# Performance work log

Hardware: AMD Instinct MI355X
Metric: run time of the kernel (lower is better)

Reference implementation:

```python
import jax, jax.numpy as jnp
import numpy as np

HEADS = 4
DIM_HEAD = 32
EPS = 1e-5


def setup_inputs() -> dict:
    key = jax.random.key(0)
    ks = jax.random.split(key, 4)
    B, dim, H, W = 8, 256, 128, 128
    hidden = HEADS * DIM_HEAD  # 128
    x = jax.random.normal(ks[0], (B, dim, H, W), dtype=jnp.float32)
    # 1x1 conv weights stored as [out_ch, in_ch]
    qkv_w = jax.random.normal(ks[1], (3 * hidden, dim), dtype=jnp.float32) * (1.0 / np.sqrt(dim))
    conv_w = jax.random.normal(ks[2], (dim, hidden), dtype=jnp.float32) * (1.0 / np.sqrt(hidden))
    conv_b = jax.random.normal(ks[3], (dim,), dtype=jnp.float32) * 0.01
    gamma = jnp.ones((dim,), dtype=jnp.float32)
    beta = jnp.zeros((dim,), dtype=jnp.float32)
    return {"x": x, "qkv_w": qkv_w, "conv_w": conv_w, "conv_b": conv_b,
            "gamma": gamma, "beta": beta}


def reference(x, qkv_w, conv_w, conv_b, gamma, beta):
    B, C, H, W = x.shape
    N = H * W
    scale = DIM_HEAD ** (-0.5)
    # qkv 1x1 conv -> [B, 3, heads, dim_head, N]
    qkv = jnp.einsum('oc,bchw->bohw', qkv_w, x).reshape(B, 3, HEADS, DIM_HEAD, N)
    q, k, v = qkv[:, 0], qkv[:, 1], qkv[:, 2]
    q = jax.nn.softmax(q, axis=-2) * scale   # softmax over dim_head axis
    k = jax.nn.softmax(k, axis=-1)           # softmax over spatial axis
    v = v / N
    # context = k @ v^T : [B, h, d, d]
    context = jnp.einsum('bhdn,bhen->bhde', k, v)
    # out = context @ q : [B, h, d, N]
    out = jnp.einsum('bhde,bhen->bhdn', context, q)
    out = out.reshape(B, HEADS * DIM_HEAD, H, W)
    # final 1x1 conv with bias
    y = jnp.einsum('oc,bchw->bohw', conv_w, out) + conv_b[None, :, None, None]
    # InstanceNorm2d(affine=True): per-sample per-channel over (H, W), biased var
    mean = jnp.mean(y, axis=(2, 3), keepdims=True)
    var = jnp.var(y, axis=(2, 3), keepdims=True)
    y = (y - mean) * jax.lax.rsqrt(var + EPS)
    return y * gamma[None, :, None, None] + beta[None, :, None, None]
```

## Files before the change

kernel.cpp:

```cpp
#include <hip/hip_runtime.h>
#include <math.h>

#define NPIX 16384
#define DIMC 256
#define BATCH 8
#define HEADS 4
#define DHEAD 32
#define HID 128
#define OQKV 384
#define EPS 1e-5f
#define SCALE 0.17677669529663687f

typedef _Float16 f16x8 __attribute__((ext_vector_type(8)));
typedef float f32x4 __attribute__((ext_vector_type(4)));

__device__ inline void gl_lds16(const void* g, void* l) {
    __builtin_amdgcn_global_load_lds(
        (const __attribute__((address_space(1))) unsigned*)g,
        (__attribute__((address_space(3))) unsigned*)l, 16, 0, 0);
}

__global__ __launch_bounds__(256) void prep_kernel(
    const float* __restrict__ qkv_w, const float* __restrict__ conv_w,
    _Float16* __restrict__ wh, _Float16* __restrict__ ch, float* __restrict__ zbuf)
{
    int i = blockIdx.x * 256 + threadIdx.x;
    if (i < 98304) wh[i] = (_Float16)qkv_w[i];
    else           ch[i - 98304] = (_Float16)conv_w[i - 98304];
    if (i < 37888) zbuf[i] = 0.f;
}

__global__ __launch_bounds__(256) void transpose_x(const float* __restrict__ x,
                                                   _Float16* __restrict__ xh)
{
    __shared__ float tile[64][65];
    int t = threadIdx.x;
    int n0 = blockIdx.x * 64;
    int c0 = blockIdx.y * 64;
    int b  = blockIdx.z;
    const float* xb = x + (long)b * DIMC * NPIX;
    #pragma unroll
    for (int it = 0; it < 4; it++) {
        int c  = it * 16 + (t >> 4);
        int n4 = (t & 15) * 4;
        float4 v = *(const float4*)&xb[(long)(c0 + c) * NPIX + n0 + n4];
        tile[c][n4] = v.x; tile[c][n4+1] = v.y; tile[c][n4+2] = v.z; tile[c][n4+3] = v.w;
    }
    __syncthreads();
    _Float16* xo = xh + (long)b * NPIX * DIMC;
    #pragma unroll
    for (int it = 0; it < 2; it++) {
        int n  = it * 32 + (t >> 3);
        int c8 = (t & 7) * 8;
        f16x8 o;
        #pragma unroll
        for (int k = 0; k < 8; k++) o[k] = (_Float16)tile[c8 + k][n];
        *(f16x8*)&xo[(long)(n0 + n) * DIMC + c0 + c8] = o;
    }
}

template<int K, int EPI>
__global__ __launch_bounds__(256) void gemm_h(
    const _Float16* __restrict__ A,
    const _Float16* __restrict__ Bm,
    _Float16* __restrict__ Cm,
    long bsB, long bsC, float* __restrict__ lnacc)
{
    __shared__ _Float16 smem[16384];
    _Float16* As = smem;
    _Float16* Bs = smem + 4096;
    const int t  = threadIdx.x;
    const int b  = blockIdx.x;
    const int m0 = blockIdx.y * 128;
    const int n0 = blockIdx.z * 128;
    const _Float16* Bb = Bm + (long)b * bsB;
    const int w = t >> 6, lane = t & 63;
    const int q = lane >> 4, l16 = lane & 15;
    const int mw = (w >> 1) * 64, nw = (w & 1) * 64;

    f32x4 acc[4][4] = {};

    for (int k0 = 0; k0 < K; k0 += 32) {
        #pragma unroll
        for (int is = 0; is < 2; is++) {
            int idx = is * 256 + t;
            int row = idx >> 2, kc = (idx & 3) * 8;
            gl_lds16(&A [(long)(m0 + row) * K + k0 + kc], &As[idx * 8]);
            gl_lds16(&Bb[(long)(n0 + row) * K + k0 + kc], &Bs[idx * 8]);
        }
        __syncthreads();
        f16x8 af[4], bf[4];
        #pragma unroll
        for (int i = 0; i < 4; i++) {
            af[i] = *(const f16x8*)&As[(mw + i * 16 + l16) * 32 + q * 8];
            bf[i] = *(const f16x8*)&Bs[(nw + i * 16 + l16) * 32 + q * 8];
        }
        #pragma unroll
        for (int i = 0; i < 4; i++)
            #pragma unroll
            for (int j = 0; j < 4; j++)
                acc[i][j] = __builtin_amdgcn_mfma_f32_16x16x32_f16(af[i], bf[j], acc[i][j], 0, 0, 0);
        __syncthreads();
    }

    _Float16* Cs = smem;
    #pragma unroll
    for (int i = 0; i < 4; i++) {
        #pragma unroll
        for (int j = 0; j < 4; j++) {
            #pragma unroll
            for (int r = 0; r < 4; r++) {
                int row = mw + i * 16 + q * 4 + r;
                int col = nw + j * 16 + l16;
                Cs[row * 128 + (col ^ ((row & 15) << 3))] = (_Float16)acc[i][j][r];
            }
        }
    }
    __syncthreads();
    _Float16* Cb = Cm + (long)b * bsC;
    #pragma unroll
    for (int it = 0; it < 8; it++) {
        int u = it * 256 + t;
        int row = u >> 4, cg = u & 15;
        f16x8 v8 = *(const f16x8*)&Cs[row * 128 + ((cg * 8) ^ ((row & 15) << 3))];
        *(f16x8*)&Cb[(long)(m0 + row) * NPIX + n0 + cg * 8] = v8;
        if (EPI) {
            float s = 0.f, sq = 0.f;
            #pragma unroll
            for (int k = 0; k < 8; k++) { float f = (float)v8[k]; s += f; sq += f * f; }
            #pragma unroll
            for (int off = 8; off > 0; off >>= 1) {
                s  += __shfl_down(s,  off, 16);
                sq += __shfl_down(sq, off, 16);
            }
            if ((t & 15) == 0) {
                int rg = b * DIMC + m0 + row;
                atomicAdd(&lnacc[rg * 2],     s);
                atomicAdd(&lnacc[rg * 2 + 1], sq);
            }
        }
    }
}

__global__ __launch_bounds__(256) void ctx_mfma(const _Float16* __restrict__ qkvh,
    float* __restrict__ ctx_raw, float* __restrict__ ksum)
{
    __shared__ float cbuf[4][1024];
    int t = threadIdx.x;
    int w = t >> 6, lane = t & 63;
    int q = lane >> 4, l16 = lane & 15;
    int bh = blockIdx.y, b = bh >> 2, h = bh & 3;
    const _Float16* kb = qkvh + ((long)b * OQKV + HID + h * DHEAD) * NPIX;
    const _Float16* vb = qkvh + ((long)b * OQKV + 2 * HID + h * DHEAD) * NPIX;
    long n0 = (long)blockIdx.x * 2048 + w * 512 + q * 8;

    f32x4 c00 = {}, c01 = {}, c10 = {}, c11 = {};
    float ks0 = 0.f, ks1 = 0.f;

    for (int s = 0; s < 16; s++) {
        long n = n0 + s * 32;
        f16x8 kf0 = *(const f16x8*)&kb[(long)l16 * NPIX + n];
        f16x8 kf1 = *(const f16x8*)&kb[(long)(16 + l16) * NPIX + n];
        f16x8 vf0 = *(const f16x8*)&vb[(long)l16 * NPIX + n];
        f16x8 vf1 = *(const f16x8*)&vb[(long)(16 + l16) * NPIX + n];
        f16x8 e0, e1;
        #pragma unroll
        for (int j = 0; j < 8; j++) {
            float ea = __expf((float)kf0[j]); e0[j] = (_Float16)ea; ks0 += ea;
            float eb = __expf((float)kf1[j]); e1[j] = (_Float16)eb; ks1 += eb;
        }
        c00 = __builtin_amdgcn_mfma_f32_16x16x32_f16(e0, vf0, c00, 0, 0, 0);
        c01 = __builtin_amdgcn_mfma_f32_16x16x32_f16(e0, vf1, c01, 0, 0, 0);
        c10 = __builtin_amdgcn_mfma_f32_16x16x32_f16(e1, vf0, c10, 0, 0, 0);
        c11 = __builtin_amdgcn_mfma_f32_16x16x32_f16(e1, vf1, c11, 0, 0, 0);
    }

    ks0 += __shfl_down(ks0, 32); ks0 += __shfl_down(ks0, 16);
    ks1 += __shfl_down(ks1, 32); ks1 += __shfl_down(ks1, 16);
    if (lane < 16) {
        atomicAdd(&ksum[bh * DHEAD + l16],      ks0);
        atomicAdd(&ksum[bh * DHEAD + 16 + l16], ks1);
    }

    float* cb = cbuf[w];
    #pragma unroll
    for (int r = 0; r < 4; r++) {
        cb[(q * 4 + r) * 32 + l16]            = c00[r];
        cb[(q * 4 + r) * 32 + 16 + l16]       = c01[r];
        cb[(16 + q * 4 + r) * 32 + l16]       = c10[r];
        cb[(16 + q * 4 + r) * 32 + 16 + l16]  = c11[r];
    }
    __syncthreads();
    #pragma unroll
    for (int ii = 0; ii < 4; ii++) {
        int idx = ii * 256 + t;
        float s = cbuf[0][idx] + cbuf[1][idx] + cbuf[2][idx] + cbuf[3][idx];
        atomicAdd(&ctx_raw[(long)bh * 1024 + idx], s);
    }
}

__global__ __launch_bounds__(256) void outq_h(_Float16* __restrict__ qkvh,
    const float* __restrict__ ctx_raw, const float* __restrict__ ksum)
{
    __shared__ float ctx_t[4][32][32];
    int tid = threadIdx.x;
    int n = blockIdx.x * 256 + tid;
    int b = blockIdx.y;
    #pragma unroll
    for (int i = 0; i < 16; i++) {
        int idx = i * 256 + tid;
        int h = idx >> 10, de = idx & 1023;
        int d = de >> 5, e = de & 31;
        float s = ksum[(b * 4 + h) * DHEAD + d];
        ctx_t[h][e][d] = SCALE * ctx_raw[(long)(b * 4 + h) * 1024 + de] / s;
    }
    __syncthreads();
    _Float16* ob = qkvh + ((long)b * OQKV + 2 * HID) * NPIX + (long)n * HID;
    for (int h = 0; h < 4; h++) {
        const _Float16* qb = qkvh + ((long)b * OQKV + h * DHEAD) * NPIX + n;
        float qv[32];
        float mx = -1e30f;
        #pragma unroll
        for (int e = 0; e < 32; e++) { qv[e] = (float)qb[(long)e * NPIX]; mx = fmaxf(mx, qv[e]); }
        float s = 0.f;
        #pragma unroll
        for (int e = 0; e < 32; e++) { qv[e] = __expf(qv[e] - mx); s += qv[e]; }
        float qs = 1.f / s;
        float4 o4[8];
        #pragma unroll
        for (int j = 0; j < 8; j++) o4[j] = make_float4(0,0,0,0);
        #pragma unroll 8
        for (int e = 0; e < 32; e++) {
            float qe = qv[e] * qs;
            #pragma unroll
            for (int j = 0; j < 8; j++) {
                float4 c = *(const float4*)&ctx_t[h][e][j * 4];
                o4[j].x += c.x * qe; o4[j].y += c.y * qe;
                o4[j].z += c.z * qe; o4[j].w += c.w * qe;
            }
        }
        #pragma unroll
        for (int j = 0; j < 4; j++) {
            f16x8 pk;
            float4 a = o4[j * 2], bb = o4[j * 2 + 1];
            pk[0] = (_Float16)a.x;  pk[1] = (_Float16)a.y;
            pk[2] = (_Float16)a.z;  pk[3] = (_Float16)a.w;
            pk[4] = (_Float16)bb.x; pk[5] = (_Float16)bb.y;
            pk[6] = (_Float16)bb.z; pk[7] = (_Float16)bb.w;
            *(f16x8*)&ob[h * DHEAD + j * 8] = pk;
        }
    }
}

__global__ __launch_bounds__(256) void ln_finalize(const float* __restrict__ lnacc,
    const float* __restrict__ gamma, const float* __restrict__ beta,
    float* __restrict__ mv)
{
    int row = blockIdx.x * 256 + threadIdx.x;
    float s = lnacc[row * 2], sq = lnacc[row * 2 + 1];
    float meanp = s * (1.f / NPIX);
    float varp  = fmaxf(sq * (1.f / NPIX) - meanp * meanp, 0.f);
    float rinv  = rsqrtf(varp * (1.f / ((float)NPIX * (float)NPIX)) + EPS);
    int c = row & 255;
    float g = rinv * gamma[c];
    mv[row * 2]     = g * (1.f / NPIX);
    mv[row * 2 + 1] = beta[c] - meanp * (1.f / NPIX) * g;
}

__global__ __launch_bounds__(256) void ln_apply(const _Float16* __restrict__ yh,
    const float* __restrict__ mv, float* __restrict__ out)
{
    long i8 = (long)blockIdx.x * 256 + threadIdx.x;
    int row = (int)(i8 >> 11);
    float a = mv[row * 2], be = mv[row * 2 + 1];
    f16x8 v = *(const f16x8*)&yh[i8 * 8];
    float4 o1, o2;
    o1.x = (float)v[0] * a + be; o1.y = (float)v[1] * a + be;
    o1.z = (float)v[2] * a + be; o1.w = (float)v[3] * a + be;
    o2.x = (float)v[4] * a + be; o2.y = (float)v[5] * a + be;
    o2.z = (float)v[6] * a + be; o2.w = (float)v[7] * a + be;
    *(float4*)&out[i8 * 8]     = o1;
    *(float4*)&out[i8 * 8 + 4] = o2;
}

extern "C" void kernel_launch(void* const* d_in, const int* in_sizes, int n_in,
                              void* d_out, int out_size, void* d_ws, size_t ws_size,
                              hipStream_t stream)
{
    const float* x      = (const float*)d_in[0];
    const float* qkv_w  = (const float*)d_in[1];
    const float* conv_w = (const float*)d_in[2];
    const float* gamma  = (const float*)d_in[4];
    const float* beta   = (const float*)d_in[5];
    float* out = (float*)d_out;

    _Float16* xh   = (_Float16*)d_ws;
    _Float16* qkvh = xh + 33554432;
    _Float16* wh   = qkvh + 50331648;
    _Float16* ch   = wh + 98304;
    float* ctx_raw = (float*)(ch + 32768);
    float* ksum    = ctx_raw + 32768;
    float* lnacc   = ksum + 1024;
    float* mv      = lnacc + 4096;
    _Float16* yh   = xh;

    prep_kernel<<<512, 256, 0, stream>>>(qkv_w, conv_w, wh, ch, ctx_raw);
    transpose_x<<<dim3(256, 4, BATCH), 256, 0, stream>>>(x, xh);
    gemm_h<256, 0><<<dim3(BATCH, 3, 128), 256, 0, stream>>>(
        wh, xh, qkvh, (long)NPIX * DIMC, (long)OQKV * NPIX, nullptr);
    ctx_mfma<<<dim3(8, 32), 256, 0, stream>>>(qkvh, ctx_raw, ksum);
    outq_h<<<dim3(64, BATCH), 256, 0, stream>>>(qkvh, ctx_raw, ksum);
    gemm_h<128, 1><<<dim3(BATCH, 2, 128), 256, 0, stream>>>(
        ch, qkvh + (long)2 * HID * NPIX, yh, (long)OQKV * NPIX, (long)DIMC * NPIX, lnacc);
    ln_finalize<<<8, 256, 0, stream>>>(lnacc, gamma, beta, mv);
    ln_apply<<<16384, 256, 0, stream>>>(yh, mv, out);
}
```

Before: 393.1 us.

## Fuse x transpose/fp16 cast into QKV GEMM reading fp32 x directly

Removes the separate transpose_x kernel that wrote an fp16 transposed copy of x, and adds a QKV GEMM that streams fp32 x tiles straight into LDS with an XOR swizzle, converting to fp16 while building MFMA B fragments. This eliminates one full write and re-read of the 64 MB fp16 activation and one kernel launch. In exchange the GEMM loads twice as many bytes per X tile (fp32), does scalar strided LDS reads plus conversions in the inner loop, and re-reads x from global once per M block (3 times).

```diff
diff --git a/kernel.cpp b/kernel.cpp
--- a/kernel.cpp
+++ b/kernel.cpp
@@ -30,32 +30,82 @@
     if (i < 37888) zbuf[i] = 0.f;
 }
 
-__global__ __launch_bounds__(256) void transpose_x(const float* __restrict__ x,
-                                                   _Float16* __restrict__ xh)
-{
-    __shared__ float tile[64][65];
-    int t = threadIdx.x;
-    int n0 = blockIdx.x * 64;
-    int c0 = blockIdx.y * 64;
-    int b  = blockIdx.z;
-    const float* xb = x + (long)b * DIMC * NPIX;
-    #pragma unroll
-    for (int it = 0; it < 4; it++) {
-        int c  = it * 16 + (t >> 4);
-        int n4 = (t & 15) * 4;
-        float4 v = *(const float4*)&xb[(long)(c0 + c) * NPIX + n0 + n4];
-        tile[c][n4] = v.x; tile[c][n4+1] = v.y; tile[c][n4+2] = v.z; tile[c][n4+3] = v.w;
+__global__ __launch_bounds__(256) void gemm_qkv(
+    const _Float16* __restrict__ A,
+    const float* __restrict__ X,
+    _Float16* __restrict__ Cm)
+{
+    __shared__ _Float16 smem[16384];
+    _Float16* As = smem;
+    float* Xs = (float*)(smem + 4096);
+    const int t  = threadIdx.x;
+    const int b  = blockIdx.x;
+    const int m0 = blockIdx.y * 128;
+    const int n0 = blockIdx.z * 128;
+    const float* Xb = X + (long)b * DIMC * NPIX;
+    const int w = t >> 6, lane = t & 63;
+    const int q = lane >> 4, l16 = lane & 15;
+    const int mw = (w >> 1) * 64, nw = (w & 1) * 64;
+    const int swzq = ((q & 1) << 4) | ((q >> 1) << 2);
+
+    f32x4 acc[4][4] = {};
+
+    for (int k0 = 0; k0 < DIMC; k0 += 32) {
+        #pragma unroll
+        for (int is = 0; is < 2; is++) {
+            int idx = is * 256 + t;
+            int row = idx >> 2, kc = (idx & 3) * 8;
+            gl_lds16(&A[(long)(m0 + row) * DIMC + k0 + kc], &As[idx * 8]);
+        }
+        #pragma unroll
+        for (int is = 0; is < 4; is++) {
+            int idx = is * 256 + t;
+            int c = idx >> 5, f4 = (idx & 31) * 4;
+            int qc = c >> 3;
+            int sw = ((qc & 1) << 4) | ((qc >> 1) << 2);
+            gl_lds16(&Xb[(long)(k0 + c) * NPIX + n0 + (f4 ^ sw)], &Xs[c * 128 + f4]);
+        }
+        __syncthreads();
+        f16x8 af[4], bf[4];
+        #pragma unroll
+        for (int i = 0; i < 4; i++)
+            af[i] = *(const f16x8*)&As[(mw + i * 16 + l16) * 32 + q * 8];
+        #pragma unroll
+        for (int i = 0; i < 4; i++) {
+            int n = nw + i * 16 + l16;
+            const float* xp = &Xs[q * 8 * 128 + (n ^ swzq)];
+            #pragma unroll
+            for (int j = 0; j < 8; j++) bf[i][j] = (_Float16)xp[j * 128];
+        }
+        #pragma unroll
+        for (int i = 0; i < 4; i++)
+            #pragma unroll
+            for (int j = 0; j < 4; j++)
+                acc[i][j] = __builtin_amdgcn_mfma_f32_16x16x32_f16(af[i], bf[j], acc[i][j], 0, 0, 0);
+        __syncthreads();
+    }
+
+    _Float16* Cs = smem;
+    #pragma unroll
+    for (int i = 0; i < 4; i++) {
+        #pragma unroll
+        for (int j = 0; j < 4; j++) {
+            #pragma unroll
+            for (int r = 0; r < 4; r++) {
+                int row = mw + i * 16 + q * 4 + r;
+                int col = nw + j * 16 + l16;
+                Cs[row * 128 + (col ^ ((row & 15) << 3))] = (_Float16)acc[i][j][r];
+            }
+        }
     }
     __syncthreads();
-    _Float16* xo = xh + (long)b * NPIX * DIMC;
-    #pragma unroll
-    for (int it = 0; it < 2; it++) {
-        int n  = it * 32 + (t >> 3);
-        int c8 = (t & 7) * 8;
-        f16x8 o;
-        #pragma unroll
-        for (int k = 0; k < 8; k++) o[k] = (_Float16)tile[c8 + k][n];
-        *(f16x8*)&xo[(long)(n0 + n) * DIMC + c0 + c8] = o;
+    _Float16* Cb = Cm + (long)b * ((long)OQKV * NPIX);
+    #pragma unroll
+    for (int it = 0; it < 8; it++) {
+        int u = it * 256 + t;
+        int row = u >> 4, cg = u & 15;
+        f16x8 v8 = *(const f16x8*)&Cs[row * 128 + ((cg * 8) ^ ((row & 15) << 3))];
+        *(f16x8*)&Cb[(long)(m0 + row) * NPIX + n0 + cg * 8] = v8;
     }
 }
 
@@ -294,20 +344,17 @@
     const float* beta   = (const float*)d_in[5];
     float* out = (float*)d_out;
 
-    _Float16* xh   = (_Float16*)d_ws;
-    _Float16* qkvh = xh + 33554432;
+    _Float16* yh   = (_Float16*)d_ws;
+    _Float16* qkvh = yh + 33554432;
     _Float16* wh   = qkvh + 50331648;
     _Float16* ch   = wh + 98304;
     float* ctx_raw = (float*)(ch + 32768);
     float* ksum    = ctx_raw + 32768;
     float* lnacc   = ksum + 1024;
     float* mv      = lnacc + 4096;
-    _Float16* yh   = xh;
 
     prep_kernel<<<512, 256, 0, stream>>>(qkv_w, conv_w, wh, ch, ctx_raw);
-    transpose_x<<<dim3(256, 4, BATCH), 256, 0, stream>>>(x, xh);
-    gemm_h<256, 0><<<dim3(BATCH, 3, 128), 256, 0, stream>>>(
-        wh, xh, qkvh, (long)NPIX * DIMC, (long)OQKV * NPIX, nullptr);
+    gemm_qkv<<<dim3(BATCH, 3, 128), 256, 0, stream>>>(wh, x, qkvh);
     ctx_mfma<<<dim3(8, 32), 256, 0, stream>>>(qkvh, ctx_raw, ksum);
     outq_h<<<dim3(64, BATCH), 256, 0, stream>>>(qkvh, ctx_raw, ksum);
     gemm_h<128, 1><<<dim3(BATCH, 2, 128), 256, 0, stream>>>(
```

New measurement: 377.4 us. 1.04x faster.
